# Kernel tuning notes

Measured on AMD Instinct MI355X. Metric: run time of the kernel, lower is better.

## Reference

```python
import jax, jax.numpy as jnp
import numpy as np
from jax import lax

MARGIN = 0.2
NMAX = 1


def setup_inputs() -> dict:
    key = jax.random.key(0)
    k1, k2 = jax.random.split(key)
    N, D = 8192, 512
    imgs = jax.random.normal(k1, (N, D), dtype=jnp.float32)
    caps = jax.random.normal(k2, (N, D), dtype=jnp.float32)
    return {"imgs": imgs, "caps": caps}


def reference(imgs, caps):
    # scores[i, j] = <img_i, cap_j>  -> [N, N]
    scores = jnp.matmul(imgs, caps.T)
    diag = jnp.diagonal(scores)  # [N]
    s = scores - 2.0 * jnp.diag(diag)
    # top-nmax over columns (axis 0): hardest negative captions per caption slot
    max_c = lax.top_k(s.T, NMAX)[0].T  # [NMAX, N]
    # top-nmax over rows (axis 1): hardest negative images per image slot
    max_i = lax.top_k(s, NMAX)[0]      # [N, NMAX]
    neg_cap = jnp.sum(jnp.maximum(max_c + (MARGIN - diag)[None, :], 0.0))
    neg_img = jnp.sum(jnp.maximum(max_i + (MARGIN - diag)[:, None], 0.0))
    return neg_cap + neg_img
```

## Files before the change

kernel.cpp:

```cpp
#include <hip/hip_runtime.h>

#define N_ROWS 8192
#define DIM    512

typedef __attribute__((ext_vector_type(4))) float frag_cd;
typedef __attribute__((ext_vector_type(4))) int   v4i;
typedef __attribute__((ext_vector_type(8))) int   v8i;

__device__ __forceinline__ unsigned f2fp8(float x) {
    float a = fabsf(x);
    unsigned s = (__float_as_uint(x) >> 31) << 7;
    if (a < 0.015625f) return s;
    a = fminf(a, 448.f);
    unsigned u = __float_as_uint(a);
    u += 0x7FFFFu + ((u >> 20) & 1u);
    unsigned exp = (u >> 23) - 120u;
    unsigned mant = (u >> 20) & 7u;
    return s | (exp << 3) | mant;
}
__device__ __forceinline__ unsigned pack4fp8(float4 v) {
    return f2fp8(v.x) | (f2fp8(v.y) << 8) | (f2fp8(v.z) << 16) | (f2fp8(v.w) << 24);
}
__device__ __forceinline__ unsigned enc_f32(float f) {
    unsigned u = __float_as_uint(f);
    return (u & 0x80000000u) ? ~u : (u | 0x80000000u);
}
__device__ __forceinline__ float dec_f32(unsigned k) {
    return __uint_as_float((k & 0x80000000u) ? (k & 0x7FFFFFFFu) : ~k);
}


__global__ __launch_bounds__(256) void k_prep(const float* __restrict__ imgs,
                                              const float* __restrict__ caps,
                                              unsigned char* __restrict__ fimgs,
                                              unsigned char* __restrict__ fcaps,
                                              float* __restrict__ diag,
                                              unsigned* __restrict__ rowmax,
                                              unsigned* __restrict__ colmax,
                                              float* __restrict__ out) {
    const int b  = blockIdx.x;
    const int cr = b >> 2;
    const int t  = threadIdx.x;
    const int w = t >> 6, l = t & 63;
    const int row = ((b & 3) << 2) + w;
    if (b == 0 && t == 0) out[0] = 0.f;
    const int r = cr * 16 + row;
    const float* ar = imgs + (size_t)r * DIM + l * 8;
    const float* br = caps + (size_t)r * DIM + l * 8;
    float4 a0 = *(const float4*)ar, a1 = *(const float4*)(ar + 4);
    float4 b0 = *(const float4*)br, b1 = *(const float4*)(br + 4);
    uint2 oa, ob;
    oa.x = pack4fp8(a0); oa.y = pack4fp8(a1);
    ob.x = pack4fp8(b0); ob.y = pack4fp8(b1);
    const size_t addr = (size_t)cr * 8192 + (size_t)((l >> 4) << 11)
                      + (((l >> 1) & 1) << 10)
                      + ((((l >> 2) & 3) << 4) + row) * 16 + ((l & 1) << 3);
    *(uint2*)(fimgs + addr) = oa;
    *(uint2*)(fcaps + addr) = ob;
    float s = a0.x * b0.x + a0.y * b0.y + a0.z * b0.z + a0.w * b0.w
            + a1.x * b1.x + a1.y * b1.y + a1.z * b1.z + a1.w * b1.w;
    #pragma unroll
    for (int m = 1; m < 64; m <<= 1) s += __shfl_xor(s, m, 64);
    if (l == 0) { diag[r] = s; rowmax[r] = 0u; colmax[r] = 0u; }
}

__global__ __launch_bounds__(256, 3) void k_gemm(const unsigned char* __restrict__ A,
                                                 const unsigned char* __restrict__ B,
                                                 unsigned* __restrict__ rowmax,
                                                 unsigned* __restrict__ colmax) {
    __shared__ unsigned char sA[2][8192];
    __shared__ unsigned char sB[2][16384];
    const int tid = threadIdx.x;
    const int w = tid >> 6, lane = tid & 63;
    const int f = (int)blockIdx.x;
    const int jb = (f & 7) * 8 + ((f >> 3) & 7);
    const int ib = f >> 6;
    const int j0 = jb << 7, i0 = ib << 6;
    const int q = lane >> 4, l15 = lane & 15;
    const int wr = (w & 1) << 5, wc = (w >> 1) << 6;

    const unsigned char* Ab = A + (size_t)(i0 >> 4) * 8192 + lane * 16;
    const unsigned char* Bb = B + (size_t)(j0 >> 4) * 8192 + lane * 16;

    frag_cd acc[2][4] = {};

    auto stage = [&](int bi, int kp2) {
        #pragma unroll
        for (int j = 0; j < 2; ++j)
            __builtin_amdgcn_global_load_lds(
                (const __attribute__((address_space(1))) unsigned int*)(Ab + (size_t)w * 8192 + kp2 * 2048 + j * 1024),
                (__attribute__((address_space(3))) unsigned int*)(&sA[bi][(w << 11) + (j << 10) + (lane << 4)]), 16, 0, 0);
        #pragma unroll
        for (int s = 0; s < 2; ++s) {
            const int ch = 2 * w + s;
            #pragma unroll
            for (int j = 0; j < 2; ++j)
                __builtin_amdgcn_global_load_lds(
                    (const __attribute__((address_space(1))) unsigned int*)(Bb + (size_t)ch * 8192 + kp2 * 2048 + j * 1024),
                    (__attribute__((address_space(3))) unsigned int*)(&sB[bi][(ch << 11) + (j << 10) + (lane << 4)]), 16, 0, 0);
        }
    };

    stage(0, 0);
    __syncthreads();

    const int u16 = lane << 4;

    #pragma unroll
    for (int kp2 = 0; kp2 < 4; ++kp2) {
        const int cur = kp2 & 1, nxt = cur ^ 1;
        if (kp2 < 3) stage(nxt, kp2 + 1);

        v8i af[2], bf[4];
        #pragma unroll
        for (int r = 0; r < 2; ++r) {
            const int ch = ((w & 1) << 1) + r;
            v4i lo = *(const v4i*)(&sA[cur][(ch << 11) + u16]);
            v4i hi = *(const v4i*)(&sA[cur][(ch << 11) + 1024 + u16]);
            v8i v;
            v[0] = lo[0]; v[1] = lo[1]; v[2] = lo[2]; v[3] = lo[3];
            v[4] = hi[0]; v[5] = hi[1]; v[6] = hi[2]; v[7] = hi[3];
            af[r] = v;
        }
        #pragma unroll
        for (int c = 0; c < 4; ++c) {
            const int ch = ((w >> 1) << 2) + c;
            v4i lo = *(const v4i*)(&sB[cur][(ch << 11) + u16]);
            v4i hi = *(const v4i*)(&sB[cur][(ch << 11) + 1024 + u16]);
            v8i v;
            v[0] = lo[0]; v[1] = lo[1]; v[2] = lo[2]; v[3] = lo[3];
            v[4] = hi[0]; v[5] = hi[1]; v[6] = hi[2]; v[7] = hi[3];
            bf[c] = v;
        }
        #pragma unroll
        for (int r = 0; r < 2; ++r)
            #pragma unroll
            for (int c = 0; c < 4; ++c)
                acc[r][c] = __builtin_amdgcn_mfma_scale_f32_16x16x128_f8f6f4(
                    af[r], bf[c], acc[r][c], 0, 0,
                    0, 0x7F7F7F7F, 0, 0x7F7F7F7F);

        __syncthreads();
    }

    const bool dblk = ((i0 >> 7) == jb);
    #pragma unroll
    for (int r = 0; r < 2; ++r)
        #pragma unroll
        for (int c = 0; c < 4; ++c)
            #pragma unroll
            for (int g = 0; g < 4; ++g) {
                float fv = acc[r][c][g];
                const int gi = wr + (r << 4) + (q << 2) + g;
                const int gj = wc + (c << 4) + l15;
                if (dblk && (i0 + gi) == (j0 + gj)) fv = -fv;
                acc[r][c][g] = fv;
            }

    #pragma unroll
    for (int r = 0; r < 2; ++r)
        #pragma unroll
        for (int g = 0; g < 4; ++g) {
            float m = fmaxf(fmaxf(acc[r][0][g], acc[r][1][g]),
                            fmaxf(acc[r][2][g], acc[r][3][g]));
            m = fmaxf(m, __shfl_xor(m, 1, 64));
            m = fmaxf(m, __shfl_xor(m, 2, 64));
            m = fmaxf(m, __shfl_xor(m, 4, 64));
            m = fmaxf(m, __shfl_xor(m, 8, 64));
            if (l15 == 0)
                atomicMax(&rowmax[i0 + wr + (r << 4) + (q << 2) + g], enc_f32(m));
        }
    #pragma unroll
    for (int c = 0; c < 4; ++c) {
        float m = acc[0][c][0];
        #pragma unroll
        for (int r = 0; r < 2; ++r)
            #pragma unroll
            for (int g = 0; g < 4; ++g) m = fmaxf(m, acc[r][c][g]);
        m = fmaxf(m, __shfl_xor(m, 16, 64));
        m = fmaxf(m, __shfl_xor(m, 32, 64));
        if (q == 0)
            atomicMax(&colmax[j0 + wc + (c << 4) + l15], enc_f32(m));
    }
}

__global__ __launch_bounds__(256) void k_final(const unsigned* __restrict__ rowmax,
                                               const unsigned* __restrict__ colmax,
                                               const float* __restrict__ diag,
                                               float* __restrict__ out) {
    const int idx = blockIdx.x * 256 + threadIdx.x;
    const float d = diag[idx];
    float s = fmaxf(dec_f32(rowmax[idx]) + 0.2f - d, 0.f)
            + fmaxf(dec_f32(colmax[idx]) + 0.2f - d, 0.f);
    #pragma unroll
    for (int m = 1; m < 64; m <<= 1) s += __shfl_xor(s, m, 64);
    __shared__ float red[4];
    if ((threadIdx.x & 63) == 0) red[threadIdx.x >> 6] = s;
    __syncthreads();
    if (threadIdx.x == 0)
        atomicAdd(out, red[0] + red[1] + red[2] + red[3]);
}

extern "C" void kernel_launch(void* const* d_in, const int* in_sizes, int n_in,
                              void* d_out, int out_size, void* d_ws, size_t ws_size,
                              hipStream_t stream) {
    const float* imgs = (const float*)d_in[0];
    const float* caps = (const float*)d_in[1];
    float* out = (float*)d_out;

    char* ws = (char*)d_ws;
    unsigned char* fimgs = (unsigned char*)ws;
    unsigned char* fcaps = (unsigned char*)(ws + 4194304);
    float*    diag   = (float*)   (ws + 8388608);
    unsigned* rowmax = (unsigned*)(ws + 8388608 + 32768);
    unsigned* colmax = (unsigned*)(ws + 8388608 + 65536);

    k_prep<<<2048, 256, 0, stream>>>(imgs, caps, fimgs, fcaps,
                                     diag, rowmax, colmax, out);
    k_gemm<<<8192, 256, 0, stream>>>(fimgs, fcaps, rowmax, colmax);
    k_final<<<N_ROWS / 256, 256, 0, stream>>>(rowmax, colmax, diag, out);
}
```

Baseline: 191.7 us.

## Drop LDS staging and load MFMA fragments directly from global with 128x128 tiles

The GEMM kernel no longer stages FP8 tiles through double-buffered shared memory. Each wave now loads its MFMA operand fragments straight from the pre-swizzled global layout. The block tile grows from 64x128 to 128x128, with a 4x4 accumulator grid per wave, which halves the grid and the number of atomic max reductions. The trade-off is that fragments are no longer shared between waves through LDS, so global/L2 traffic rises, there is no explicit prefetch overlap, and register pressure goes up (launch bounds lowered to 2 blocks).

```diff
diff --git a/kernel.cpp b/kernel.cpp
--- a/kernel.cpp
+++ b/kernel.cpp
@@ -64,88 +64,51 @@
     if (l == 0) { diag[r] = s; rowmax[r] = 0u; colmax[r] = 0u; }
 }
 
-__global__ __launch_bounds__(256, 3) void k_gemm(const unsigned char* __restrict__ A,
+__global__ __launch_bounds__(256, 2) void k_gemm(const unsigned char* __restrict__ A,
                                                  const unsigned char* __restrict__ B,
                                                  unsigned* __restrict__ rowmax,
                                                  unsigned* __restrict__ colmax) {
-    __shared__ unsigned char sA[2][8192];
-    __shared__ unsigned char sB[2][16384];
     const int tid = threadIdx.x;
     const int w = tid >> 6, lane = tid & 63;
     const int f = (int)blockIdx.x;
     const int jb = (f & 7) * 8 + ((f >> 3) & 7);
     const int ib = f >> 6;
-    const int j0 = jb << 7, i0 = ib << 6;
+    const int j0 = jb << 7, i0 = ib << 7;
     const int q = lane >> 4, l15 = lane & 15;
-    const int wr = (w & 1) << 5, wc = (w >> 1) << 6;
+    const int wr = (w & 1) << 6, wc = (w >> 1) << 6;
 
-    const unsigned char* Ab = A + (size_t)(i0 >> 4) * 8192 + lane * 16;
-    const unsigned char* Bb = B + (size_t)(j0 >> 4) * 8192 + lane * 16;
+    const unsigned char* Ab = A + (size_t)((i0 >> 4) + ((w & 1) << 2)) * 8192 + lane * 16;
+    const unsigned char* Bb = B + (size_t)((j0 >> 4) + ((w >> 1) << 2)) * 8192 + lane * 16;
 
-    frag_cd acc[2][4] = {};
+    frag_cd acc[4][4] = {};
 
-    auto stage = [&](int bi, int kp2) {
-        #pragma unroll
-        for (int j = 0; j < 2; ++j)
-            __builtin_amdgcn_global_load_lds(
-                (const __attribute__((address_space(1))) unsigned int*)(Ab + (size_t)w * 8192 + kp2 * 2048 + j * 1024),
-                (__attribute__((address_space(3))) unsigned int*)(&sA[bi][(w << 11) + (j << 10) + (lane << 4)]), 16, 0, 0);
-        #pragma unroll
-        for (int s = 0; s < 2; ++s) {
-            const int ch = 2 * w + s;
-            #pragma unroll
-            for (int j = 0; j < 2; ++j)
-                __builtin_amdgcn_global_load_lds(
-                    (const __attribute__((address_space(1))) unsigned int*)(Bb + (size_t)ch * 8192 + kp2 * 2048 + j * 1024),
-                    (__attribute__((address_space(3))) unsigned int*)(&sB[bi][(ch << 11) + (j << 10) + (lane << 4)]), 16, 0, 0);
-        }
-    };
-
-    stage(0, 0);
-    __syncthreads();
-
-    const int u16 = lane << 4;
+    union U { v8i v; struct { v4i lo, hi; } s; };
 
     #pragma unroll
     for (int kp2 = 0; kp2 < 4; ++kp2) {
-        const int cur = kp2 & 1, nxt = cur ^ 1;
-        if (kp2 < 3) stage(nxt, kp2 + 1);
-
-        v8i af[2], bf[4];
+        U af[4], bf[4];
         #pragma unroll
-        for (int r = 0; r < 2; ++r) {
-            const int ch = ((w & 1) << 1) + r;
-            v4i lo = *(const v4i*)(&sA[cur][(ch << 11) + u16]);
-            v4i hi = *(const v4i*)(&sA[cur][(ch << 11) + 1024 + u16]);
-            v8i v;
-            v[0] = lo[0]; v[1] = lo[1]; v[2] = lo[2]; v[3] = lo[3];
-            v[4] = hi[0]; v[5] = hi[1]; v[6] = hi[2]; v[7] = hi[3];
-            af[r] = v;
+        for (int r = 0; r < 4; ++r) {
+            af[r].s.lo = *(const v4i*)(Ab + (size_t)r * 8192 + kp2 * 2048);
+            af[r].s.hi = *(const v4i*)(Ab + (size_t)r * 8192 + kp2 * 2048 + 1024);
         }
         #pragma unroll
         for (int c = 0; c < 4; ++c) {
-            const int ch = ((w >> 1) << 2) + c;
-            v4i lo = *(const v4i*)(&sB[cur][(ch << 11) + u16]);
-            v4i hi = *(const v4i*)(&sB[cur][(ch << 11) + 1024 + u16]);
-            v8i v;
-            v[0] = lo[0]; v[1] = lo[1]; v[2] = lo[2]; v[3] = lo[3];
-            v[4] = hi[0]; v[5] = hi[1]; v[6] = hi[2]; v[7] = hi[3];
-            bf[c] = v;
+            bf[c].s.lo = *(const v4i*)(Bb + (size_t)c * 8192 + kp2 * 2048);
+            bf[c].s.hi = *(const v4i*)(Bb + (size_t)c * 8192 + kp2 * 2048 + 1024);
         }
         #pragma unroll
-        for (int r = 0; r < 2; ++r)
+        for (int r = 0; r < 4; ++r)
             #pragma unroll
             for (int c = 0; c < 4; ++c)
                 acc[r][c] = __builtin_amdgcn_mfma_scale_f32_16x16x128_f8f6f4(
-                    af[r], bf[c], acc[r][c], 0, 0,
+                    af[r].v, bf[c].v, acc[r][c], 0, 0,
                     0, 0x7F7F7F7F, 0, 0x7F7F7F7F);
-
-        __syncthreads();
     }
 
-    const bool dblk = ((i0 >> 7) == jb);
+    const bool dblk = (i0 == j0);
     #pragma unroll
-    for (int r = 0; r < 2; ++r)
+    for (int r = 0; r < 4; ++r)
         #pragma unroll
         for (int c = 0; c < 4; ++c)
             #pragma unroll
@@ -158,7 +121,7 @@
             }
 
     #pragma unroll
-    for (int r = 0; r < 2; ++r)
+    for (int r = 0; r < 4; ++r)
         #pragma unroll
         for (int g = 0; g < 4; ++g) {
             float m = fmaxf(fmaxf(acc[r][0][g], acc[r][1][g]),
@@ -174,7 +137,7 @@
     for (int c = 0; c < 4; ++c) {
         float m = acc[0][c][0];
         #pragma unroll
-        for (int r = 0; r < 2; ++r)
+        for (int r = 0; r < 4; ++r)
             #pragma unroll
             for (int g = 0; g < 4; ++g) m = fmaxf(m, acc[r][c][g]);
         m = fmaxf(m, __shfl_xor(m, 16, 64));
@@ -217,6 +180,6 @@
 
     k_prep<<<2048, 256, 0, stream>>>(imgs, caps, fimgs, fcaps,
                                      diag, rowmax, colmax, out);
-    k_gemm<<<8192, 256, 0, stream>>>(fimgs, fcaps, rowmax, colmax);
+    k_gemm<<<4096, 256, 0, stream>>>(fimgs, fcaps, rowmax, colmax);
     k_final<<<N_ROWS / 256, 256, 0, stream>>>(rowmax, colmax, diag, out);
 }
```

Result: faster. 175.9 us (-8.2%).
